# Kernel tuning notes

Measured on AMD Instinct MI355X. Metric: run time of the kernel, lower is better.

Reference implementation:

```python
import jax, jax.numpy as jnp
import numpy as np

N, F, D, K, B, L, E, H = 12288, 128, 128, 3, 64, 256, 393216, 8
DT = 2 * D  # token dim
ALPHA = 0.5


def _mlp(h, w1, b1, w2, b2):
    return jax.nn.relu(h @ w1 + b1) @ w2 + b2


def setup_inputs() -> dict:
    key = jax.random.key(0)
    ks = jax.random.split(key, 24)
    s = 0.05
    x = jax.random.normal(ks[0], (N, F), jnp.float32)
    proj_w = jax.random.normal(ks[1], (F, D), jnp.float32) * s
    proj_b = jnp.zeros((D,), jnp.float32)
    adj_rows = jax.random.randint(ks[2], (E,), 0, N, jnp.int32)
    adj_cols = jax.random.randint(ks[3], (E,), 0, N, jnp.int32)
    adj_vals = jax.random.uniform(ks[4], (E,), jnp.float32) / 32.0
    ppr = jax.random.uniform(ks[5], (N, N), jnp.float32) * 0.01
    drnl = jax.random.uniform(ks[6], (B, N), jnp.float32) * 10.0
    src = jax.random.randint(ks[7], (B,), 0, N, jnp.int32)
    dst = jax.random.randint(ks[8], (B,), 0, N, jnp.int32)
    sample_idx = jnp.repeat(jnp.arange(B, dtype=jnp.int32), L)
    node_idx = jax.random.randint(ks[9], (B, L), 0, N, jnp.int32)
    node_idx = node_idx.at[:, 0].set(src).at[:, 1].set(dst).reshape(-1)
    enc_w1 = jax.random.normal(ks[10], (4, 2, D), jnp.float32) * 0.2
    enc_b1 = jnp.zeros((4, D), jnp.float32)
    enc_w2 = jax.random.normal(ks[11], (4, D, D), jnp.float32) * s
    enc_b2 = jnp.zeros((4, D), jnp.float32)
    struct_w1 = jax.random.normal(ks[12], (4 * D, D), jnp.float32) * s
    struct_b1 = jnp.zeros((D,), jnp.float32)
    struct_w2 = jax.random.normal(ks[13], (D, D), jnp.float32) * s
    struct_b2 = jnp.zeros((D,), jnp.float32)
    cls_tok = jax.random.normal(ks[14], (DT,), jnp.float32) * s
    wq = jax.random.normal(ks[15], (DT, DT), jnp.float32) * s
    wk = jax.random.normal(ks[16], (DT, DT), jnp.float32) * s
    wv = jax.random.normal(ks[17], (DT, DT), jnp.float32) * s
    wo = jax.random.normal(ks[18], (DT, DT), jnp.float32) * s
    return dict(x=x, proj_w=proj_w, proj_b=proj_b, adj_vals=adj_vals,
                adj_rows=adj_rows, adj_cols=adj_cols, ppr=ppr, drnl=drnl,
                src=src, dst=dst, sample_idx=sample_idx, node_idx=node_idx,
                enc_w1=enc_w1, enc_b1=enc_b1, enc_w2=enc_w2, enc_b2=enc_b2,
                struct_w1=struct_w1, struct_b1=struct_b1, struct_w2=struct_w2,
                struct_b2=struct_b2, cls_tok=cls_tok, wq=wq, wk=wk, wv=wv, wo=wo)


def reference(x, proj_w, proj_b, adj_vals, adj_rows, adj_cols, ppr, drnl,
              src, dst, sample_idx, node_idx,
              enc_w1, enc_b1, enc_w2, enc_b2,
              struct_w1, struct_b1, struct_w2, struct_b2,
              cls_tok, wq, wk, wv, wo):
    # --- re_features: feature_proj + K sparse matmul hops, APPNP-style mix ---
    feats = x @ proj_w + proj_b                      # [N, D]
    h = feats
    for _ in range(K):
        h = jax.ops.segment_sum(adj_vals[:, None] * h[adj_cols], adj_rows,
                                num_segments=N)      # sparse adj @ h
    re_x = h * (1.0 - ALPHA) + feats * ALPHA         # [N, D]

    # --- cal_heuristic: dense ppr row gather + drnl lookup ---
    n = sample_idx.shape[0]
    ppr_a = ppr[src[sample_idx], node_idx]           # [n]
    ppr_b = ppr[dst[sample_idx], node_idx]
    drnl_v = drnl[sample_idx, node_idx]
    heur = jnp.zeros((n, 4, 2), jnp.float32)
    heur = heur.at[:, 2, 0].set(ppr_a).at[:, 2, 1].set(ppr_b)
    heur = heur.at[:, 3, 0].set(drnl_v).at[:, 3, 1].set(drnl_v)

    # --- tokenizer: 4 heuristic MLPs -> structure MLP, concat node feats ---
    enc = jax.vmap(_mlp)(heur.transpose(1, 0, 2), enc_w1, enc_b1, enc_w2, enc_b2)
    struct_in = enc.transpose(1, 0, 2).reshape(n, 4 * D)   # [n, 4D] (CN,AA,PPR,DRNL)
    struct = _mlp(struct_in, struct_w1, struct_b1, struct_w2, struct_b2)  # [n, D]
    tok = jnp.concatenate([struct, re_x[node_idx]], axis=-1).reshape(B, L, DT)

    # --- GraphTransformer: CLS + multi-head self-attention ---
    cls = jnp.broadcast_to(cls_tok, (B, 1, DT))
    seq = jnp.concatenate([cls, tok], axis=1)        # [B, L+1, DT]
    dh = DT // H
    q = (seq @ wq).reshape(B, L + 1, H, dh)
    k = (seq @ wk).reshape(B, L + 1, H, dh)
    v = (seq @ wv).reshape(B, L + 1, H, dh)
    att = jax.nn.softmax(jnp.einsum('bqhd,bkhd->bhqk', q, k) / jnp.sqrt(jnp.float32(dh)), axis=-1)
    out = jnp.einsum('bhqk,bkhd->bqhd', att, v).reshape(B, L + 1, DT) @ wo
    h_cls, h_a, h_b = out[:, 0], out[:, 1], out[:, 2]
    return jnp.concatenate([h_a, h_b, h_cls], axis=-1)  # [B, 6*dim]
```

## Files before the change

kernel.cpp:

```cpp
#include <hip/hip_runtime.h>
#include <math.h>

#define NN 12288
#define FD 128
#define DD 128
#define EE 393216
#define BB 64
#define LL 256
#define HH 8
#define DTD 256
#define NTOK 16384
#define CAP 128

#define PROJ_B0 1536
#define PREP_B0 1728
#define HEUR_B0 2816
#define SBIAS_B 2880
#define CLS_B   2881
#define SETUP_GRID 2882

#define SEQ_ST 272
#define STG_ST 272

typedef float f32x4 __attribute__((ext_vector_type(4)));
typedef short s16x8 __attribute__((ext_vector_type(8)));

__device__ __forceinline__ float relu_(float x){ return fmaxf(x, 0.0f); }

__device__ __forceinline__ unsigned short f2b(float f){
  unsigned int u = __float_as_uint(f);
  u += 0x7FFFu + ((u >> 16) & 1u);
  return (unsigned short)(u >> 16);
}
__device__ __forceinline__ float b2f(unsigned short h){
  return __uint_as_float(((unsigned int)h) << 16);
}

__device__ __forceinline__ f32x4 MF(s16x8 a, s16x8 b, f32x4 c){
  return __builtin_amdgcn_mfma_f32_16x16x32_bf16(a, b, c, 0, 0, 0);
}

__global__ void __launch_bounds__(256)
k_setup(const float* __restrict__ x, const float* __restrict__ proj_w,
        const float* __restrict__ proj_b, unsigned short* __restrict__ featsb,
        const float* __restrict__ wq, const float* __restrict__ wk,
        const float* __restrict__ wv,
        const float* __restrict__ enc_w2, const float* __restrict__ sw1,
        const float* __restrict__ sw2, const float* __restrict__ cls_tok,
        unsigned short* __restrict__ wqT, unsigned short* __restrict__ wkT,
        unsigned short* __restrict__ wvT,
        unsigned short* __restrict__ w2T2, unsigned short* __restrict__ w2T3,
        unsigned short* __restrict__ sw1aT, unsigned short* __restrict__ sw1bT,
        unsigned short* __restrict__ sw2T,
        const int* __restrict__ node_idx, const int* __restrict__ srcI,
        const int* __restrict__ dstI, const float* __restrict__ ppr,
        const float* __restrict__ drnl, float* __restrict__ heurA,
        float* __restrict__ heurB, float* __restrict__ heurD,
        const int* __restrict__ adj_rows, const int* __restrict__ adj_cols,
        const float* __restrict__ adj_vals, int* __restrict__ cnt,
        uint2* __restrict__ ccv,
        const float* __restrict__ enc_b1, const float* __restrict__ enc_b2,
        const float* __restrict__ sb1, float* __restrict__ sbias,
        float* __restrict__ qcls, unsigned short* __restrict__ kcls,
        unsigned short* __restrict__ vcls){
  int t = threadIdx.x;
  if(blockIdx.x < PROJ_B0){
    int e = blockIdx.x*256 + t;
    int r = adj_rows[e];
    int p = atomicAdd(&cnt[r], 1);
    ccv[(size_t)r*CAP + p] = make_uint2((unsigned)adj_cols[e], __float_as_uint(adj_vals[e]));
  } else if(blockIdx.x < PREP_B0){
    int bid = blockIdx.x - PROJ_B0;
    int row0 = bid * 64;
    int lane = t & 63, w = t >> 6;
    int lr = lane & 15, lg = lane >> 4;
    f32x4 acc[4][2];
    #pragma unroll
    for(int nt=0;nt<2;++nt){
      int col = w*32 + nt*16 + lr;
      float bv = proj_b[col];
      #pragma unroll
      for(int rt=0;rt<4;++rt)
        #pragma unroll
        for(int i=0;i<4;++i) acc[rt][nt][i]=bv;
    }
    #pragma unroll
    for(int ks=0; ks<4; ++ks){
      int kb = ks*32 + lg*8;
      s16x8 Bf[2];
      #pragma unroll
      for(int nt=0;nt<2;++nt){
        int col = w*32 + nt*16 + lr;
        #pragma unroll
        for(int i=0;i<8;++i) Bf[nt][i] = (short)f2b(proj_w[(kb+i)*DD + col]);
      }
      #pragma unroll
      for(int rt=0;rt<4;++rt){
        int row = row0 + rt*16 + lr;
        const f32x4* xp = (const f32x4*)(x + (size_t)row*FD + kb);
        f32x4 v0 = xp[0], v1 = xp[1];
        s16x8 Af;
        #pragma unroll
        for(int i=0;i<4;++i){ Af[i] = (short)f2b(v0[i]); Af[4+i] = (short)f2b(v1[i]); }
        #pragma unroll
        for(int nt=0;nt<2;++nt) acc[rt][nt] = MF(Af, Bf[nt], acc[rt][nt]);
      }
    }
    #pragma unroll
    for(int rt=0;rt<4;++rt)
      #pragma unroll
      for(int nt=0;nt<2;++nt)
        #pragma unroll
        for(int i=0;i<4;++i){
          int row = row0 + rt*16 + lg*4 + i;
          int col = w*32 + nt*16 + lr;
          featsb[(size_t)row*DD + col] = f2b(acc[rt][nt][i]);
        }
  } else if(blockIdx.x < HEUR_B0){
    int id = (blockIdx.x - PREP_B0)*256 + t;
    if(id < 196608){
      int m = id >> 16, e = id & 65535;
      int n = e & 255, k = e >> 8;
      const float* s = (m==0)? wq : (m==1)? wk : wv;
      unsigned short* d = (m==0)? wqT : (m==1)? wkT : wvT;
      d[n*256 + k] = f2b(s[k*256 + n]);
    } else {
      int id2 = id - 196608;
      int m = id2 >> 14, e = id2 & 16383;
      int n = e & 127, k = e >> 7;
      const float* s;
      unsigned short* d;
      if(m==0){ s = enc_w2 + 2*16384; d = w2T2; }
      else if(m==1){ s = enc_w2 + 3*16384; d = w2T3; }
      else if(m==2){ s = sw1 + 256*128; d = sw1aT; }
      else if(m==3){ s = sw1 + 384*128; d = sw1bT; }
      else { s = sw2; d = sw2T; }
      d[n*128 + k] = f2b(s[k*128 + n]);
    }
  } else if(blockIdx.x < SBIAS_B){
    int tt = (blockIdx.x - HEUR_B0)*256 + t;
    int s = tt >> 8;
    int node = node_idx[tt];
    heurA[tt] = ppr[(size_t)srcI[s]*NN + node];
    heurB[tt] = ppr[(size_t)dstI[s]*NN + node];
    heurD[tt] = drnl[(size_t)s*NN + node];
  } else if(blockIdx.x == SBIAS_B){
    __shared__ float h0[DD], h1[DD], e0[DD], e1[DD];
    if(t < DD){
      h0[t] = relu_(enc_b1[0*DD+t]);
      h1[t] = relu_(enc_b1[1*DD+t]);
    }
    __syncthreads();
    if(t < DD){
      float a0 = enc_b2[0*DD+t], a1 = enc_b2[1*DD+t];
      for(int d=0; d<DD; ++d){
        a0 += h0[d]*enc_w2[(0*DD+d)*DD + t];
        a1 += h1[d]*enc_w2[(1*DD+d)*DD + t];
      }
      e0[t]=a0; e1[t]=a1;
    }
    __syncthreads();
    if(t < DD){
      float sv = sb1[t];
      for(int d=0; d<DD; ++d)
        sv += e0[d]*sw1[d*DD + t] + e1[d]*sw1[(DD+d)*DD + t];
      sbias[t]=sv;
    }
  } else {
    __shared__ float scls[DTD];
    scls[t] = cls_tok[t];
    __syncthreads();
    float aq=0.f, ak=0.f, av=0.f;
    for(int d=0; d<DTD; ++d){
      float cv = scls[d];
      aq += cv*wq[d*DTD + t];
      ak += cv*wk[d*DTD + t];
      av += cv*wv[d*DTD + t];
    }
    qcls[t] = aq;
    kcls[t] = f2b(ak);
    vcls[t] = f2b(av);
  }
}

__global__ void __launch_bounds__(256)
k_spmm_w(const unsigned int* __restrict__ hin32, unsigned int* __restrict__ hout32,
         const int* __restrict__ cnt, const uint2* __restrict__ ccv,
         const unsigned int* __restrict__ featsb32, int finalpass){
  int lane = threadIdx.x & 63;
  int r = blockIdx.x*4 + (threadIdx.x>>6);
  int deg = cnt[r];
  const uint2* base = ccv + (size_t)r*CAP;
  float a0=0.f,a1=0.f,b0=0.f,b1=0.f,c0=0.f,c1=0.f,d0=0.f,d1=0.f;
  int p = 0;
  for(; p+4 <= deg; p += 4){
    uint2 q0 = base[p], q1 = base[p+1], q2 = base[p+2], q3 = base[p+3];
    unsigned u0 = hin32[(size_t)q0.x*64 + lane];
    unsigned u1 = hin32[(size_t)q1.x*64 + lane];
    unsigned u2 = hin32[(size_t)q2.x*64 + lane];
    unsigned u3 = hin32[(size_t)q3.x*64 + lane];
    float v0=__uint_as_float(q0.y), v1=__uint_as_float(q1.y);
    float v2=__uint_as_float(q2.y), v3=__uint_as_float(q3.y);
    a0 += v0*b2f((unsigned short)(u0&0xffffu)); a1 += v0*b2f((unsigned short)(u0>>16));
    b0 += v1*b2f((unsigned short)(u1&0xffffu)); b1 += v1*b2f((unsigned short)(u1>>16));
    c0 += v2*b2f((unsigned short)(u2&0xffffu)); c1 += v2*b2f((unsigned short)(u2>>16));
    d0 += v3*b2f((unsigned short)(u3&0xffffu)); d1 += v3*b2f((unsigned short)(u3>>16));
  }
  for(; p < deg; ++p){
    uint2 q0 = base[p];
    unsigned u0 = hin32[(size_t)q0.x*64 + lane];
    float v0 = __uint_as_float(q0.y);
    a0 += v0*b2f((unsigned short)(u0&0xffffu)); a1 += v0*b2f((unsigned short)(u0>>16));
  }
  a0 += b0 + c0 + d0;
  a1 += b1 + c1 + d1;
  if(finalpass){
    unsigned f = featsb32[(size_t)r*64 + lane];
    a0 = 0.5f*a0 + 0.5f*b2f((unsigned short)(f & 0xffffu));
    a1 = 0.5f*a1 + 0.5f*b2f((unsigned short)(f >> 16));
  }
  hout32[(size_t)r*64 + lane] = (unsigned)f2b(a0) | ((unsigned)f2b(a1) << 16);
}

__global__ void __launch_bounds__(256)
k_tok_kv(const int* __restrict__ node_idx,
         const float* __restrict__ heurA, const float* __restrict__ heurB,
         const float* __restrict__ heurD,
         const float* __restrict__ enc_w1, const float* __restrict__ enc_b1,
         const unsigned short* __restrict__ w2T2, const unsigned short* __restrict__ w2T3,
         const float* __restrict__ enc_b2,
         const unsigned short* __restrict__ sw1aT, const unsigned short* __restrict__ sw1bT,
         const float* __restrict__ sbias,
         const unsigned short* __restrict__ sw2T, const float* __restrict__ sb2,
         const unsigned short* __restrict__ rexb,
         const unsigned short* __restrict__ wkT, const unsigned short* __restrict__ wvT,
         const unsigned short* __restrict__ wqT,
         unsigned short* __restrict__ kbuf, unsigned short* __restrict__ vbuf,
         float* __restrict__ qbuf){
  __shared__ float sA[64], sB[64], sDV[64];
  __shared__ int sNode[64];
  __shared__ __align__(16) unsigned short hid[64*136];
  __shared__ __align__(16) unsigned short uni[64*STG_ST];
  unsigned short* pe2 = uni;
  unsigned short* pe3 = uni + 64*136;
  unsigned short* seq = uni;
  unsigned short* stg = uni;

  int tid = threadIdx.x;
  int lane = tid & 63;
  int w = tid >> 6;
  int lr = lane & 15;
  int lg = lane >> 4;
  int t0 = blockIdx.x * 64;
  int bs = t0 >> 8;
  int p0 = t0 & 255;

  if(tid < 64){
    int tt = t0 + tid;
    sNode[tid] = node_idx[tt];
    sA[tid]  = heurA[tt];
    sB[tid]  = heurB[tt];
    sDV[tid] = heurD[tt];
  }
  __syncthreads();

  {
    f32x4 acc2[4][2], acc3[4][2];
    #pragma unroll
    for(int nt=0;nt<2;++nt){
      int col = w*32 + nt*16 + lr;
      float b2v = enc_b2[2*DD + col];
      float b3v = enc_b2[3*DD + col];
      #pragma unroll
      for(int rt=0;rt<4;++rt)
        #pragma unroll
        for(int i=0;i<4;++i){ acc2[rt][nt][i]=b2v; acc3[rt][nt][i]=b3v; }
    }
    #pragma unroll
    for(int ks=0; ks<4; ++ks){
      int kb = ks*32 + lg*8;
      float w20[8], w21[8], w3s[8], b2c[8], b3c[8];
      #pragma unroll
      for(int i=0;i<8;++i){
        int k = kb + i;
        w20[i] = enc_w1[4*DD + k];
        w21[i] = enc_w1[5*DD + k];
        w3s[i] = enc_w1[6*DD + k] + enc_w1[7*DD + k];
        b2c[i] = enc_b1[2*DD + k];
        b3c[i] = enc_b1[3*DD + k];
      }
      s16x8 B2[2], B3[2];
      #pragma unroll
      for(int nt=0;nt<2;++nt){
        int col = w*32 + nt*16 + lr;
        B2[nt] = *(const s16x8*)(w2T2 + col*DD + kb);
        B3[nt] = *(const s16x8*)(w2T3 + col*DD + kb);
      }
      #pragma unroll
      for(int rt=0;rt<4;++rt){
        int row = rt*16 + lr;
        float a = sA[row], b = sB[row], dv = sDV[row];
        s16x8 A2, A3;
        #pragma unroll
        for(int i=0;i<8;++i){
          A2[i] = (short)f2b(relu_(a*w20[i] + b*w21[i] + b2c[i]));
          A3[i] = (short)f2b(relu_(dv*w3s[i] + b3c[i]));
        }
        #pragma unroll
        for(int nt=0;nt<2;++nt){
          acc2[rt][nt] = MF(A2, B2[nt], acc2[rt][nt]);
          acc3[rt][nt] = MF(A3, B3[nt], acc3[rt][nt]);
        }
      }
    }
    #pragma unroll
    for(int rt=0;rt<4;++rt)
      #pragma unroll
      for(int nt=0;nt<2;++nt)
        #pragma unroll
        for(int i=0;i<4;++i){
          int row = rt*16 + lg*4 + i;
          int col = w*32 + nt*16 + lr;
          pe2[row*136 + col] = f2b(acc2[rt][nt][i]);
          pe3[row*136 + col] = f2b(acc3[rt][nt][i]);
        }
  }
  __syncthreads();

  {
    f32x4 acc[4][2];
    #pragma unroll
    for(int nt=0;nt<2;++nt){
      int col = w*32 + nt*16 + lr;
      float sv = sbias[col];
      #pragma unroll
      for(int rt=0;rt<4;++rt)
        #pragma unroll
        for(int i=0;i<4;++i) acc[rt][nt][i]=sv;
    }
    #pragma unroll
    for(int ks=0; ks<4; ++ks){
      int kb = ks*32 + lg*8;
      s16x8 Ba[2], Bb[2];
      #pragma unroll
      for(int nt=0;nt<2;++nt){
        int col = w*32 + nt*16 + lr;
        Ba[nt] = *(const s16x8*)(sw1aT + col*DD + kb);
        Bb[nt] = *(const s16x8*)(sw1bT + col*DD + kb);
      }
      #pragma unroll
      for(int rt=0;rt<4;++rt){
        s16x8 A2 = *(const s16x8*)&pe2[(rt*16+lr)*136 + kb];
        s16x8 A3 = *(const s16x8*)&pe3[(rt*16+lr)*136 + kb];
        #pragma unroll
        for(int nt=0;nt<2;++nt){
          acc[rt][nt] = MF(A2, Ba[nt], acc[rt][nt]);
          acc[rt][nt] = MF(A3, Bb[nt], acc[rt][nt]);
        }
      }
    }
    __syncthreads();
    #pragma unroll
    for(int rt=0;rt<4;++rt)
      #pragma unroll
      for(int nt=0;nt<2;++nt)
        #pragma unroll
        for(int i=0;i<4;++i){
          int row = rt*16 + lg*4 + i;
          int col = w*32 + nt*16 + lr;
          hid[row*136 + col] = f2b(relu_(acc[rt][nt][i]));
        }
  }
  __syncthreads();

  {
    f32x4 acc[4][2];
    #pragma unroll
    for(int nt=0;nt<2;++nt){
      int col = w*32 + nt*16 + lr;
      float bv = sb2[col];
      #pragma unroll
      for(int rt=0;rt<4;++rt)
        #pragma unroll
        for(int i=0;i<4;++i) acc[rt][nt][i]=bv;
    }
    #pragma unroll
    for(int ks=0; ks<4; ++ks){
      int kb = ks*32 + lg*8;
      s16x8 Bc[2];
      #pragma unroll
      for(int nt=0;nt<2;++nt){
        int col = w*32 + nt*16 + lr;
        Bc[nt] = *(const s16x8*)(sw2T + col*DD + kb);
      }
      #pragma unroll
      for(int rt=0;rt<4;++rt){
        s16x8 A = *(const s16x8*)&hid[(rt*16+lr)*136 + kb];
        #pragma unroll
        for(int nt=0;nt<2;++nt) acc[rt][nt] = MF(A, Bc[nt], acc[rt][nt]);
      }
    }
    #pragma unroll
    for(int rt=0;rt<4;++rt)
      #pragma unroll
      for(int nt=0;nt<2;++nt)
        #pragma unroll
        for(int i=0;i<4;++i){
          int row = rt*16 + lg*4 + i;
          int col = w*32 + nt*16 + lr;
          seq[row*SEQ_ST + col] = f2b(acc[rt][nt][i]);
        }
    int row = tid >> 2, l4 = tid & 3;
    int c = l4 * 32;
    int node = sNode[row];
    const unsigned short* rp = rexb + (size_t)node*DD + c;
    #pragma unroll
    for(int j=0;j<4;++j)
      *(s16x8*)(seq + row*SEQ_ST + DD + c + j*8) = *(const s16x8*)(rp + j*8);
  }
  __syncthreads();

  f32x4 accK[4][4], accV[4][4];
  {
    #pragma unroll
    for(int rt=0;rt<4;++rt)
      #pragma unroll
      for(int nt=0;nt<4;++nt)
        #pragma unroll
        for(int i=0;i<4;++i){ accK[rt][nt][i]=0.f; accV[rt][nt][i]=0.f; }
    int col0 = w * 64;
    #pragma unroll
    for(int ks=0; ks<8; ++ks){
      int kb = ks*32 + lg*8;
      s16x8 A[4], Bk[4], Bv[4];
      #pragma unroll
      for(int rt=0;rt<4;++rt)
        A[rt] = *(const s16x8*)&seq[(rt*16+lr)*SEQ_ST + kb];
      #pragma unroll
      for(int nt=0;nt<4;++nt){
        int col = col0 + nt*16 + lr;
        Bk[nt] = *(const s16x8*)(wkT + (size_t)col*DTD + kb);
        Bv[nt] = *(const s16x8*)(wvT + (size_t)col*DTD + kb);
      }
      #pragma unroll
      for(int rt=0;rt<4;++rt)
        #pragma unroll
        for(int nt=0;nt<4;++nt){
          accK[rt][nt] = MF(A[rt], Bk[nt], accK[rt][nt]);
          accV[rt][nt] = MF(A[rt], Bv[nt], accV[rt][nt]);
        }
    }
  }
  if(p0 == 0){
    #pragma unroll
    for(int qi=0; qi<2; ++qi){
      int col = w*64 + lane;
      float acc = 0.f;
      for(int d=0; d<DTD; d+=8){
        s16x8 wv8 = *(const s16x8*)(wqT + (size_t)col*DTD + d);
        #pragma unroll
        for(int j=0;j<8;++j)
          acc += b2f(seq[qi*SEQ_ST + d + j]) * b2f((unsigned short)wv8[j]);
      }
      qbuf[(size_t)(bs*2+qi)*DTD + col] = acc;
    }
  }
  __syncthreads();

  {
    int col0 = w * 64;
    #pragma unroll
    for(int rt=0;rt<4;++rt)
      #pragma unroll
      for(int nt=0;nt<4;++nt)
        #pragma unroll
        for(int i=0;i<4;++i)
          stg[(rt*16 + lg*4 + i)*STG_ST + col0 + nt*16 + lr] = f2b(accK[rt][nt][i]);
  }
  __syncthreads();
  {
    int row = tid >> 2, c = (tid & 3)*64;
    #pragma unroll
    for(int j=0;j<8;++j)
      *(s16x8*)(kbuf + (size_t)(t0+row)*DTD + c + j*8) = *(const s16x8*)&stg[row*STG_ST + c + j*8];
  }
  __syncthreads();
  {
    int col0 = w * 64;
    #pragma unroll
    for(int rt=0;rt<4;++rt)
      #pragma unroll
      for(int nt=0;nt<4;++nt)
        #pragma unroll
        for(int i=0;i<4;++i)
          stg[(rt*16 + lg*4 + i)*STG_ST + col0 + nt*16 + lr] = f2b(accV[rt][nt][i]);
  }
  __syncthreads();
  {
    int row = tid >> 2, c = (tid & 3)*64;
    #pragma unroll
    for(int j=0;j<8;++j)
      *(s16x8*)(vbuf + (size_t)(t0+row)*DTD + c + j*8) = *(const s16x8*)&stg[row*STG_ST + c + j*8];
  }
}

__global__ void __launch_bounds__(256)
k_att2(const float* __restrict__ qcls, const float* __restrict__ qbuf,
       const unsigned short* __restrict__ kcls, const unsigned short* __restrict__ vcls,
       const unsigned short* __restrict__ kbuf, const unsigned short* __restrict__ vbuf,
       float* __restrict__ att_o){
  __shared__ float q_s[3][32];
  __shared__ float sc[3][257];
  __shared__ float ppv[8][3][32];
  int t = threadIdx.x;
  int b = blockIdx.x >> 3, h = blockIdx.x & 7;

  if(t < 96){
    int qi = t>>5, dd = t&31;
    q_s[qi][dd] = (qi==0) ? qcls[h*32 + dd]
                          : qbuf[(size_t)(b*2+qi-1)*DTD + h*32 + dd];
  }
  __syncthreads();
  const float scale = 0.17677669529663687f;
  for(int kk=t; kk<257; kk+=256){
    const unsigned short* kr = (kk==0) ? (kcls + h*32)
                                       : (kbuf + (size_t)(b*256+kk-1)*DTD + h*32);
    float kv[32];
    #pragma unroll
    for(int j=0;j<4;++j){
      s16x8 u = *(const s16x8*)(kr + j*8);
      #pragma unroll
      for(int m2=0;m2<8;++m2) kv[j*8+m2] = b2f((unsigned short)u[m2]);
    }
    float d0=0.f,d1=0.f,d2=0.f;
    #pragma unroll
    for(int dd=0;dd<32;++dd){
      d0 += q_s[0][dd]*kv[dd]; d1 += q_s[1][dd]*kv[dd]; d2 += q_s[2][dd]*kv[dd];
    }
    sc[0][kk]=d0*scale; sc[1][kk]=d1*scale; sc[2][kk]=d2*scale;
  }
  __syncthreads();
  {
    int wv = t>>6, lane = t&63;
    if(wv < 3){
      int qi = wv;
      float x0=sc[qi][lane], x1=sc[qi][lane+64], x2=sc[qi][lane+128], x3=sc[qi][lane+192];
      float x4 = (lane==0)? sc[qi][256] : -1e30f;
      float m = fmaxf(fmaxf(fmaxf(x0,x1),fmaxf(x2,x3)),x4);
      #pragma unroll
      for(int off=32; off>0; off>>=1) m = fmaxf(m, __shfl_xor(m, off));
      float e0=expf(x0-m), e1=expf(x1-m), e2v=expf(x2-m), e3v=expf(x3-m);
      float e4=(lane==0)? expf(x4-m) : 0.f;
      float s = e0+e1+e2v+e3v+e4;
      #pragma unroll
      for(int off=32; off>0; off>>=1) s += __shfl_xor(s, off);
      float inv = 1.0f/s;
      sc[qi][lane]=e0*inv; sc[qi][lane+64]=e1*inv;
      sc[qi][lane+128]=e2v*inv; sc[qi][lane+192]=e3v*inv;
      if(lane==0) sc[qi][256]=e4*inv;
    }
  }
  __syncthreads();
  {
    int dd = t & 31, g = t >> 5;
    float a0=0.f, a1=0.f, a2=0.f;
    for(int kk=g; kk<257; kk+=8){
      const unsigned short* vr = (kk==0) ? (vcls + h*32)
                                         : (vbuf + (size_t)(b*256+kk-1)*DTD + h*32);
      float v = b2f(vr[dd]);
      a0 += sc[0][kk]*v; a1 += sc[1][kk]*v; a2 += sc[2][kk]*v;
    }
    ppv[g][0][dd]=a0; ppv[g][1][dd]=a1; ppv[g][2][dd]=a2;
  }
  __syncthreads();
  if(t < 96){
    int qi = t>>5, dd = t&31;
    float s = 0.f;
    #pragma unroll
    for(int gg=0; gg<8; ++gg) s += ppv[gg][qi][dd];
    att_o[(size_t)(b*3+qi)*DTD + h*32 + dd] = s;
  }
}

__global__ void k_out(const float* __restrict__ att_o, const float* __restrict__ wo,
                      float* __restrict__ out){
  __shared__ float srow[DTD];
  int t = threadIdx.x;
  int r = blockIdx.x;
  int b = r/3, qi = r - b*3;
  srow[t] = att_o[(size_t)r*DTD + t];
  __syncthreads();
  float acc = 0.f;
  for(int d=0; d<DTD; ++d) acc += srow[d]*wo[d*DTD + t];
  int off = (qi==1)? 0 : ((qi==2)? DTD : 2*DTD);
  out[(size_t)b*768 + off + t] = acc;
}

extern "C" void kernel_launch(void* const* d_in, const int* in_sizes, int n_in,
                              void* d_out, int out_size, void* d_ws, size_t ws_size,
                              hipStream_t stream){
  const float* x        = (const float*)d_in[0];
  const float* proj_w   = (const float*)d_in[1];
  const float* proj_b   = (const float*)d_in[2];
  const float* adj_vals = (const float*)d_in[3];
  const int*   adj_rows = (const int*)d_in[4];
  const int*   adj_cols = (const int*)d_in[5];
  const float* ppr      = (const float*)d_in[6];
  const float* drnl     = (const float*)d_in[7];
  const int*   srcI     = (const int*)d_in[8];
  const int*   dstI     = (const int*)d_in[9];
  const int*   node_idx   = (const int*)d_in[11];
  const float* enc_w1   = (const float*)d_in[12];
  const float* enc_b1   = (const float*)d_in[13];
  const float* enc_w2   = (const float*)d_in[14];
  const float* enc_b2   = (const float*)d_in[15];
  const float* sw1      = (const float*)d_in[16];
  const float* sb1      = (const float*)d_in[17];
  const float* sw2      = (const float*)d_in[18];
  const float* sb2      = (const float*)d_in[19];
  const float* cls_tok  = (const float*)d_in[20];
  const float* wq       = (const float*)d_in[21];
  const float* wk       = (const float*)d_in[22];
  const float* wv       = (const float*)d_in[23];
  const float* wo       = (const float*)d_in[24];
  float* out = (float*)d_out;

  char* p = (char*)d_ws;
  auto alloc = [&](size_t bytes)->void*{ void* r = (void*)p; p += (bytes + 63) & ~(size_t)63; return r; };
  unsigned short* featsb = (unsigned short*)alloc((size_t)NN*DD*2);
  unsigned short* h1b    = (unsigned short*)alloc((size_t)NN*DD*2);
  unsigned short* h2b    = (unsigned short*)alloc((size_t)NN*DD*2);
  unsigned short* rexb   = (unsigned short*)alloc((size_t)NN*DD*2);
  int*   cnt     = (int*)  alloc((size_t)NN*4);
  uint2* ccv     = (uint2*)alloc((size_t)NN*CAP*8);
  float* sbias   = (float*)alloc((size_t)DD*4);
  float* heurA   = (float*)alloc((size_t)NTOK*4);
  float* heurB   = (float*)alloc((size_t)NTOK*4);
  float* heurD   = (float*)alloc((size_t)NTOK*4);
  unsigned short* kbuf = (unsigned short*)alloc((size_t)NTOK*DTD*2);
  unsigned short* vbuf = (unsigned short*)alloc((size_t)NTOK*DTD*2);
  float* qbuf    = (float*)alloc((size_t)BB*2*DTD*4);
  float* qcls    = (float*)alloc((size_t)DTD*4);
  unsigned short* kcls = (unsigned short*)alloc((size_t)DTD*2);
  unsigned short* vcls = (unsigned short*)alloc((size_t)DTD*2);
  float* att_o   = (float*)alloc((size_t)BB*3*DTD*4);
  unsigned short* wqT   = (unsigned short*)alloc((size_t)DTD*DTD*2);
  unsigned short* wkT   = (unsigned short*)alloc((size_t)DTD*DTD*2);
  unsigned short* wvT   = (unsigned short*)alloc((size_t)DTD*DTD*2);
  unsigned short* w2T2  = (unsigned short*)alloc((size_t)DD*DD*2);
  unsigned short* w2T3  = (unsigned short*)alloc((size_t)DD*DD*2);
  unsigned short* sw1aT = (unsigned short*)alloc((size_t)DD*DD*2);
  unsigned short* sw1bT = (unsigned short*)alloc((size_t)DD*DD*2);
  unsigned short* sw2T  = (unsigned short*)alloc((size_t)DD*DD*2);

  hipMemsetAsync(cnt, 0, NN*sizeof(int), stream);

  k_setup  <<<SETUP_GRID, 256, 0, stream>>>(x, proj_w, proj_b, featsb,
                                            wq, wk, wv, enc_w2, sw1, sw2, cls_tok,
                                            wqT, wkT, wvT, w2T2, w2T3, sw1aT, sw1bT, sw2T,
                                            node_idx, srcI, dstI, ppr, drnl,
                                            heurA, heurB, heurD,
                                            adj_rows, adj_cols, adj_vals, cnt, ccv,
                                            enc_b1, enc_b2, sb1, sbias,
                                            qcls, kcls, vcls);
  k_spmm_w <<<NN/4,   256, 0, stream>>>((const unsigned*)featsb, (unsigned*)h1b, cnt, ccv, (const unsigned*)featsb, 0);
  k_spmm_w <<<NN/4,   256, 0, stream>>>((const unsigned*)h1b, (unsigned*)h2b, cnt, ccv, (const unsigned*)featsb, 0);
  k_spmm_w <<<NN/4,   256, 0, stream>>>((const unsigned*)h2b, (unsigned*)rexb, cnt, ccv, (const unsigned*)featsb, 1);
  k_tok_kv <<<NTOK/64,256, 0, stream>>>(node_idx, heurA, heurB, heurD,
                                        enc_w1, enc_b1, w2T2, w2T3, enc_b2,
                                        sw1aT, sw1bT, sbias, sw2T, sb2, rexb,
                                        wkT, wvT, wqT, kbuf, vbuf, qbuf);
  k_att2   <<<BB*HH,  256, 0, stream>>>(qcls, qbuf, kcls, vcls, kbuf, vbuf, att_o);
  k_out    <<<BB*3,   256, 0, stream>>>(att_o, wo, out);
}
```

Measured before the change: 155.7 us.

## Double k_tok_kv waves to 8 per block and tile weight transposes through LDS

The token/KV kernel now runs 512 threads (8 waves) per block, each wave covering half as many output columns, so per-thread MFMA accumulators shrink and more waves hide latency. The weight-transpose section of the setup kernel now moves 64x64 tiles through shared memory, which replaces element-wise strided writes with coalesced ones and cuts the block count for that section. The trade-off is more waves sharing each block's LDS and barriers, and possibly lower occupancy per CU.

```diff
diff --git a/kernel.cpp b/kernel.cpp
--- a/kernel.cpp
+++ b/kernel.cpp
@@ -14,10 +14,10 @@
 
 #define PROJ_B0 1536
 #define PREP_B0 1728
-#define HEUR_B0 2816
-#define SBIAS_B 2880
-#define CLS_B   2881
-#define SETUP_GRID 2882
+#define HEUR_B0 1796
+#define SBIAS_B 1860
+#define CLS_B   1861
+#define SETUP_GRID 1862
 
 #define SEQ_ST 272
 #define STG_ST 272
@@ -117,25 +117,35 @@
           featsb[(size_t)row*DD + col] = f2b(acc[rt][nt][i]);
         }
   } else if(blockIdx.x < HEUR_B0){
-    int id = (blockIdx.x - PREP_B0)*256 + t;
-    if(id < 196608){
-      int m = id >> 16, e = id & 65535;
-      int n = e & 255, k = e >> 8;
-      const float* s = (m==0)? wq : (m==1)? wk : wv;
-      unsigned short* d = (m==0)? wqT : (m==1)? wkT : wvT;
-      d[n*256 + k] = f2b(s[k*256 + n]);
+    int bid = blockIdx.x - PREP_B0;
+    const float* s; unsigned short* d; int S, k0, n0;
+    if(bid < 48){
+      int m = bid >> 4, t16 = bid & 15;
+      s = (m==0)? wq : (m==1)? wk : wv;
+      d = (m==0)? wqT : (m==1)? wkT : wvT;
+      S = 256; k0 = (t16>>2)*64; n0 = (t16&3)*64;
     } else {
-      int id2 = id - 196608;
-      int m = id2 >> 14, e = id2 & 16383;
-      int n = e & 127, k = e >> 7;
-      const float* s;
-      unsigned short* d;
+      int b2 = bid - 48; int m = b2 >> 2, t4 = b2 & 3;
       if(m==0){ s = enc_w2 + 2*16384; d = w2T2; }
       else if(m==1){ s = enc_w2 + 3*16384; d = w2T3; }
       else if(m==2){ s = sw1 + 256*128; d = sw1aT; }
       else if(m==3){ s = sw1 + 384*128; d = sw1bT; }
       else { s = sw2; d = sw2T; }
-      d[n*128 + k] = f2b(s[k*128 + n]);
+      S = 128; k0 = (t4>>1)*64; n0 = (t4&1)*64;
+    }
+    __shared__ unsigned short tile[64][65];
+    #pragma unroll
+    for(int it=0; it<16; ++it){
+      int idx = t + it*256;
+      int i = idx>>6, j = idx&63;
+      tile[i][j] = f2b(s[(size_t)(k0+i)*S + n0 + j]);
+    }
+    __syncthreads();
+    #pragma unroll
+    for(int it=0; it<16; ++it){
+      int idx = t + it*256;
+      int i2 = idx>>6, j2 = idx&63;
+      d[(size_t)(n0+i2)*S + k0 + j2] = tile[j2][i2];
     }
   } else if(blockIdx.x < SBIAS_B){
     int tt = (blockIdx.x - HEUR_B0)*256 + t;
@@ -153,17 +163,17 @@
     __syncthreads();
     if(t < DD){
       float a0 = enc_b2[0*DD+t], a1 = enc_b2[1*DD+t];
-      for(int d=0; d<DD; ++d){
-        a0 += h0[d]*enc_w2[(0*DD+d)*DD + t];
-        a1 += h1[d]*enc_w2[(1*DD+d)*DD + t];
+      for(int d2=0; d2<DD; ++d2){
+        a0 += h0[d2]*enc_w2[(0*DD+d2)*DD + t];
+        a1 += h1[d2]*enc_w2[(1*DD+d2)*DD + t];
       }
       e0[t]=a0; e1[t]=a1;
     }
     __syncthreads();
     if(t < DD){
       float sv = sb1[t];
-      for(int d=0; d<DD; ++d)
-        sv += e0[d]*sw1[d*DD + t] + e1[d]*sw1[(DD+d)*DD + t];
+      for(int d2=0; d2<DD; ++d2)
+        sv += e0[d2]*sw1[d2*DD + t] + e1[d2]*sw1[(DD+d2)*DD + t];
       sbias[t]=sv;
     }
   } else {
@@ -171,11 +181,11 @@
     scls[t] = cls_tok[t];
     __syncthreads();
     float aq=0.f, ak=0.f, av=0.f;
-    for(int d=0; d<DTD; ++d){
-      float cv = scls[d];
-      aq += cv*wq[d*DTD + t];
-      ak += cv*wk[d*DTD + t];
-      av += cv*wv[d*DTD + t];
+    for(int d2=0; d2<DTD; ++d2){
+      float cv = scls[d2];
+      aq += cv*wq[d2*DTD + t];
+      ak += cv*wk[d2*DTD + t];
+      av += cv*wv[d2*DTD + t];
     }
     qcls[t] = aq;
     kcls[t] = f2b(ak);
@@ -222,7 +232,7 @@
   hout32[(size_t)r*64 + lane] = (unsigned)f2b(a0) | ((unsigned)f2b(a1) << 16);
 }
 
-__global__ void __launch_bounds__(256)
+__global__ void __launch_bounds__(512)
 k_tok_kv(const int* __restrict__ node_idx,
          const float* __restrict__ heurA, const float* __restrict__ heurB,
          const float* __restrict__ heurD,
@@ -264,18 +274,16 @@
   }
   __syncthreads();
 
-  {
-    f32x4 acc2[4][2], acc3[4][2];
-    #pragma unroll
-    for(int nt=0;nt<2;++nt){
-      int col = w*32 + nt*16 + lr;
-      float b2v = enc_b2[2*DD + col];
-      float b3v = enc_b2[3*DD + col];
-      #pragma unroll
-      for(int rt=0;rt<4;++rt)
-        #pragma unroll
-        for(int i=0;i<4;++i){ acc2[rt][nt][i]=b2v; acc3[rt][nt][i]=b3v; }
-    }
+  int colm = w*16 + lr;
+
+  {
+    f32x4 acc2[4], acc3[4];
+    float b2v = enc_b2[2*DD + colm];
+    float b3v = enc_b2[3*DD + colm];
+    #pragma unroll
+    for(int rt=0;rt<4;++rt)
+      #pragma unroll
+      for(int i=0;i<4;++i){ acc2[rt][i]=b2v; acc3[rt][i]=b3v; }
     #pragma unroll
     for(int ks=0; ks<4; ++ks){
       int kb = ks*32 + lg*8;
@@ -289,13 +297,8 @@
         b2c[i] = enc_b1[2*DD + k];
         b3c[i] = enc_b1[3*DD + k];
       }
-      s16x8 B2[2], B3[2];
-      #pragma unroll
-      for(int nt=0;nt<2;++nt){
-        int col = w*32 + nt*16 + lr;
-        B2[nt] = *(const s16x8*)(w2T2 + col*DD + kb);
-        B3[nt] = *(const s16x8*)(w2T3 + col*DD + kb);
-      }
+      s16x8 B2 = *(const s16x8*)(w2T2 + colm*DD + kb);
+      s16x8 B3 = *(const s16x8*)(w2T3 + colm*DD + kb);
       #pragma unroll
       for(int rt=0;rt<4;++rt){
         int row = rt*16 + lr;
@@ -306,138 +309,102 @@
           A2[i] = (short)f2b(relu_(a*w20[i] + b*w21[i] + b2c[i]));
           A3[i] = (short)f2b(relu_(dv*w3s[i] + b3c[i]));
         }
-        #pragma unroll
-        for(int nt=0;nt<2;++nt){
-          acc2[rt][nt] = MF(A2, B2[nt], acc2[rt][nt]);
-          acc3[rt][nt] = MF(A3, B3[nt], acc3[rt][nt]);
-        }
-      }
-    }
-    #pragma unroll
-    for(int rt=0;rt<4;++rt)
-      #pragma unroll
-      for(int nt=0;nt<2;++nt)
-        #pragma unroll
-        for(int i=0;i<4;++i){
-          int row = rt*16 + lg*4 + i;
-          int col = w*32 + nt*16 + lr;
-          pe2[row*136 + col] = f2b(acc2[rt][nt][i]);
-          pe3[row*136 + col] = f2b(acc3[rt][nt][i]);
-        }
-  }
-  __syncthreads();
-
-  {
-    f32x4 acc[4][2];
-    #pragma unroll
-    for(int nt=0;nt<2;++nt){
-      int col = w*32 + nt*16 + lr;
-      float sv = sbias[col];
-      #pragma unroll
-      for(int rt=0;rt<4;++rt)
-        #pragma unroll
-        for(int i=0;i<4;++i) acc[rt][nt][i]=sv;
-    }
+        acc2[rt] = MF(A2, B2, acc2[rt]);
+        acc3[rt] = MF(A3, B3, acc3[rt]);
+      }
+    }
+    #pragma unroll
+    for(int rt=0;rt<4;++rt)
+      #pragma unroll
+      for(int i=0;i<4;++i){
+        int row = rt*16 + lg*4 + i;
+        pe2[row*136 + colm] = f2b(acc2[rt][i]);
+        pe3[row*136 + colm] = f2b(acc3[rt][i]);
+      }
+  }
+  __syncthreads();
+
+  {
+    f32x4 acc[4];
+    float sv = sbias[colm];
+    #pragma unroll
+    for(int rt=0;rt<4;++rt)
+      #pragma unroll
+      for(int i=0;i<4;++i) acc[rt][i]=sv;
     #pragma unroll
     for(int ks=0; ks<4; ++ks){
       int kb = ks*32 + lg*8;
-      s16x8 Ba[2], Bb[2];
-      #pragma unroll
-      for(int nt=0;nt<2;++nt){
-        int col = w*32 + nt*16 + lr;
-        Ba[nt] = *(const s16x8*)(sw1aT + col*DD + kb);
-        Bb[nt] = *(const s16x8*)(sw1bT + col*DD + kb);
-      }
+      s16x8 Ba = *(const s16x8*)(sw1aT + colm*DD + kb);
+      s16x8 Bb = *(const s16x8*)(sw1bT + colm*DD + kb);
       #pragma unroll
       for(int rt=0;rt<4;++rt){
         s16x8 A2 = *(const s16x8*)&pe2[(rt*16+lr)*136 + kb];
         s16x8 A3 = *(const s16x8*)&pe3[(rt*16+lr)*136 + kb];
-        #pragma unroll
-        for(int nt=0;nt<2;++nt){
-          acc[rt][nt] = MF(A2, Ba[nt], acc[rt][nt]);
-          acc[rt][nt] = MF(A3, Bb[nt], acc[rt][nt]);
-        }
+        acc[rt] = MF(A2, Ba, acc[rt]);
+        acc[rt] = MF(A3, Bb, acc[rt]);
       }
     }
     __syncthreads();
     #pragma unroll
     for(int rt=0;rt<4;++rt)
       #pragma unroll
-      for(int nt=0;nt<2;++nt)
-        #pragma unroll
-        for(int i=0;i<4;++i){
-          int row = rt*16 + lg*4 + i;
-          int col = w*32 + nt*16 + lr;
-          hid[row*136 + col] = f2b(relu_(acc[rt][nt][i]));
-        }
-  }
-  __syncthreads();
-
-  {
-    f32x4 acc[4][2];
-    #pragma unroll
-    for(int nt=0;nt<2;++nt){
-      int col = w*32 + nt*16 + lr;
-      float bv = sb2[col];
-      #pragma unroll
-      for(int rt=0;rt<4;++rt)
-        #pragma unroll
-        for(int i=0;i<4;++i) acc[rt][nt][i]=bv;
-    }
+      for(int i=0;i<4;++i){
+        int row = rt*16 + lg*4 + i;
+        hid[row*136 + colm] = f2b(relu_(acc[rt][i]));
+      }
+  }
+  __syncthreads();
+
+  {
+    f32x4 acc[4];
+    float bv = sb2[colm];
+    #pragma unroll
+    for(int rt=0;rt<4;++rt)
+      #pragma unroll
+      for(int i=0;i<4;++i) acc[rt][i]=bv;
     #pragma unroll
     for(int ks=0; ks<4; ++ks){
       int kb = ks*32 + lg*8;
-      s16x8 Bc[2];
-      #pragma unroll
-      for(int nt=0;nt<2;++nt){
-        int col = w*32 + nt*16 + lr;
-        Bc[nt] = *(const s16x8*)(sw2T + col*DD + kb);
-      }
+      s16x8 Bc = *(const s16x8*)(sw2T + colm*DD + kb);
       #pragma unroll
       for(int rt=0;rt<4;++rt){
         s16x8 A = *(const s16x8*)&hid[(rt*16+lr)*136 + kb];
-        #pragma unroll
-        for(int nt=0;nt<2;++nt) acc[rt][nt] = MF(A, Bc[nt], acc[rt][nt]);
-      }
-    }
-    #pragma unroll
-    for(int rt=0;rt<4;++rt)
-      #pragma unroll
-      for(int nt=0;nt<2;++nt)
-        #pragma unroll
-        for(int i=0;i<4;++i){
-          int row = rt*16 + lg*4 + i;
-          int col = w*32 + nt*16 + lr;
-          seq[row*SEQ_ST + col] = f2b(acc[rt][nt][i]);
-        }
-    int row = tid >> 2, l4 = tid & 3;
-    int c = l4 * 32;
+        acc[rt] = MF(A, Bc, acc[rt]);
+      }
+    }
+    #pragma unroll
+    for(int rt=0;rt<4;++rt)
+      #pragma unroll
+      for(int i=0;i<4;++i){
+        int row = rt*16 + lg*4 + i;
+        seq[row*SEQ_ST + colm] = f2b(acc[rt][i]);
+      }
+    int row = tid >> 3, c = (tid & 7)*16;
     int node = sNode[row];
     const unsigned short* rp = rexb + (size_t)node*DD + c;
-    #pragma unroll
-    for(int j=0;j<4;++j)
-      *(s16x8*)(seq + row*SEQ_ST + DD + c + j*8) = *(const s16x8*)(rp + j*8);
-  }
-  __syncthreads();
-
-  f32x4 accK[4][4], accV[4][4];
-  {
-    #pragma unroll
-    for(int rt=0;rt<4;++rt)
-      #pragma unroll
-      for(int nt=0;nt<4;++nt)
+    *(s16x8*)(seq + row*SEQ_ST + DD + c)     = *(const s16x8*)(rp);
+    *(s16x8*)(seq + row*SEQ_ST + DD + c + 8) = *(const s16x8*)(rp + 8);
+  }
+  __syncthreads();
+
+  f32x4 accK[4][2], accV[4][2];
+  {
+    #pragma unroll
+    for(int rt=0;rt<4;++rt)
+      #pragma unroll
+      for(int nt=0;nt<2;++nt)
         #pragma unroll
         for(int i=0;i<4;++i){ accK[rt][nt][i]=0.f; accV[rt][nt][i]=0.f; }
-    int col0 = w * 64;
+    int col0 = w * 32;
     #pragma unroll
     for(int ks=0; ks<8; ++ks){
       int kb = ks*32 + lg*8;
-      s16x8 A[4], Bk[4], Bv[4];
+      s16x8 A[4], Bk[2], Bv[2];
       #pragma unroll
       for(int rt=0;rt<4;++rt)
         A[rt] = *(const s16x8*)&seq[(rt*16+lr)*SEQ_ST + kb];
       #pragma unroll
-      for(int nt=0;nt<4;++nt){
+      for(int nt=0;nt<2;++nt){
         int col = col0 + nt*16 + lr;
         Bk[nt] = *(const s16x8*)(wkT + (size_t)col*DTD + kb);
         Bv[nt] = *(const s16x8*)(wvT + (size_t)col*DTD + kb);
@@ -445,61 +412,58 @@
       #pragma unroll
       for(int rt=0;rt<4;++rt)
         #pragma unroll
-        for(int nt=0;nt<4;++nt){
+        for(int nt=0;nt<2;++nt){
           accK[rt][nt] = MF(A[rt], Bk[nt], accK[rt][nt]);
           accV[rt][nt] = MF(A[rt], Bv[nt], accV[rt][nt]);
         }
     }
   }
   if(p0 == 0){
-    #pragma unroll
-    for(int qi=0; qi<2; ++qi){
-      int col = w*64 + lane;
-      float acc = 0.f;
-      for(int d=0; d<DTD; d+=8){
-        s16x8 wv8 = *(const s16x8*)(wqT + (size_t)col*DTD + d);
-        #pragma unroll
-        for(int j=0;j<8;++j)
-          acc += b2f(seq[qi*SEQ_ST + d + j]) * b2f((unsigned short)wv8[j]);
-      }
-      qbuf[(size_t)(bs*2+qi)*DTD + col] = acc;
-    }
-  }
-  __syncthreads();
-
-  {
-    int col0 = w * 64;
-    #pragma unroll
-    for(int rt=0;rt<4;++rt)
-      #pragma unroll
-      for(int nt=0;nt<4;++nt)
+    int qi = tid >> 8, col = tid & 255;
+    float acc = 0.f;
+    for(int d=0; d<DTD; d+=8){
+      s16x8 wv8 = *(const s16x8*)(wqT + (size_t)col*DTD + d);
+      #pragma unroll
+      for(int j=0;j<8;++j)
+        acc += b2f(seq[qi*SEQ_ST + d + j]) * b2f((unsigned short)wv8[j]);
+    }
+    qbuf[(size_t)(bs*2+qi)*DTD + col] = acc;
+  }
+  __syncthreads();
+
+  {
+    int col0 = w * 32;
+    #pragma unroll
+    for(int rt=0;rt<4;++rt)
+      #pragma unroll
+      for(int nt=0;nt<2;++nt)
         #pragma unroll
         for(int i=0;i<4;++i)
           stg[(rt*16 + lg*4 + i)*STG_ST + col0 + nt*16 + lr] = f2b(accK[rt][nt][i]);
   }
   __syncthreads();
   {
-    int row = tid >> 2, c = (tid & 3)*64;
-    #pragma unroll
-    for(int j=0;j<8;++j)
+    int row = tid >> 3, c = (tid & 7)*32;
+    #pragma unroll
+    for(int j=0;j<4;++j)
       *(s16x8*)(kbuf + (size_t)(t0+row)*DTD + c + j*8) = *(const s16x8*)&stg[row*STG_ST + c + j*8];
   }
   __syncthreads();
   {
-    int col0 = w * 64;
-    #pragma unroll
-    for(int rt=0;rt<4;++rt)
-      #pragma unroll
-      for(int nt=0;nt<4;++nt)
+    int col0 = w * 32;
+    #pragma unroll
+    for(int rt=0;rt<4;++rt)
+      #pragma unroll
+      for(int nt=0;nt<2;++nt)
         #pragma unroll
         for(int i=0;i<4;++i)
           stg[(rt*16 + lg*4 + i)*STG_ST + col0 + nt*16 + lr] = f2b(accV[rt][nt][i]);
   }
   __syncthreads();
   {
-    int row = tid >> 2, c = (tid & 3)*64;
-    #pragma unroll
-    for(int j=0;j<8;++j)
+    int row = tid >> 3, c = (tid & 7)*32;
+    #pragma unroll
+    for(int j=0;j<4;++j)
       *(s16x8*)(vbuf + (size_t)(t0+row)*DTD + c + j*8) = *(const s16x8*)&stg[row*STG_ST + c + j*8];
   }
 }
@@ -666,7 +630,7 @@
   k_spmm_w <<<NN/4,   256, 0, stream>>>((const unsigned*)featsb, (unsigned*)h1b, cnt, ccv, (const unsigned*)featsb, 0);
   k_spmm_w <<<NN/4,   256, 0, stream>>>((const unsigned*)h1b, (unsigned*)h2b, cnt, ccv, (const unsigned*)featsb, 0);
   k_spmm_w <<<NN/4,   256, 0, stream>>>((const unsigned*)h2b, (unsigned*)rexb, cnt, ccv, (const unsigned*)featsb, 1);
-  k_tok_kv <<<NTOK/64,256, 0, stream>>>(node_idx, heurA, heurB, heurD,
+  k_tok_kv <<<NTOK/64,512, 0, stream>>>(node_idx, heurA, heurB, heurD,
                                         enc_w1, enc_b1, w2T2, w2T3, enc_b2,
                                         sw1aT, sw1bT, sbias, sw2T, sb2, rexb,
                                         wkT, wvT, wqT, kbuf, vbuf, qbuf);
```

Result: no change. 154.2 us (-1.0%).
